# Optimization experiments

Hardware: AMD Instinct MI355X
Metric: run time of the kernel (lower is better)

## Reference

```python
import jax, jax.numpy as jnp
import numpy as np


def _cayley():
    # Cl(3,0) basis blades ordered by grade, lexicographic: 1,e1,e2,e3,e12,e13,e23,e123
    blades = [0b000, 0b001, 0b010, 0b100, 0b011, 0b101, 0b110, 0b111]
    idx = {b: i for i, b in enumerate(blades)}
    C = np.zeros((8, 8, 8), np.float32)
    for a in blades:
        for b in blades:
            t, s = a >> 1, 0
            while t:
                s += bin(t & b).count('1')
                t >>= 1
            C[idx[a], idx[a ^ b], idx[b]] = -1.0 if (s & 1) else 1.0
    return jnp.asarray(C)

CAYLEY = _cayley()                      # [8,8,8], metric [1,1,1]
GRADE = jnp.array([0, 1, 1, 1, 2, 2, 2, 3])  # blade -> grade (subspace) index
N_NODES, N_EDGES = 5, 20
NUM_HEADS = 8


def mv_linear(x, w, b):
    # MVLinear with subspaces=True: one scalar weight per (out, in, grade),
    # expanded to the 8 blades; bias only on the grade-0 (scalar) blade.
    # x: [N, m, 8], w: [n, m, 4], b: [n]
    out = jnp.einsum('bmi,nmi->bni', x, w[:, :, GRADE])
    return out.at[..., 0].add(b)


def _ln(x, g, b):
    m = jnp.mean(x, axis=-1, keepdims=True)
    v = jnp.var(x, axis=-1, keepdims=True)
    return (x - m) * jax.lax.rsqrt(v + 1e-5) * g + b


def _forward(nodes, edges, src_mask, batch_size, W_in, b_in, W_gp, b_gp,
             Wq, Wk, Wv, Wo, ln1_g, ln1_b, ln2_g, ln2_b, W1, b1, W2, b2):
    B = batch_size
    S = N_NODES + N_EDGES
    c_in = nodes.shape[1]
    nodes4 = nodes.reshape(B, N_NODES, c_in, 8)
    edges4 = edges.reshape(B, N_EDGES, c_in, 8)
    src = jnp.concatenate([nodes4, edges4], axis=1).reshape(B * S, c_in, 8)

    src_mv = mv_linear(src, W_in, b_in)                               # [B*S, dm, 8]
    src_gp = jnp.einsum('bni,ijk,bnk->bnj', src_mv, CAYLEY, src_mv)   # geometric product
    src2 = mv_linear(jnp.concatenate([src_mv, src_gp], axis=1), W_gp, b_gp)

    dm = src2.shape[1]
    D = dm * 8                                                        # 56 flat features
    H = NUM_HEADS
    hd = D // H
    x = src2.reshape(B, S, D)

    L = Wq.shape[0]
    for l in range(L):                                                # fixed small layer count
        h = _ln(x, ln1_g[l], ln1_b[l])
        q = (h @ Wq[l]).reshape(B, S, H, hd)
        k = (h @ Wk[l]).reshape(B, S, H, hd)
        v = (h @ Wv[l]).reshape(B, S, H, hd)
        scores = jnp.einsum('bqhd,bkhd->bhqk', q, k) / jnp.sqrt(jnp.float32(hd))
        scores = scores + src_mask[:, None, :, :]
        attn = jax.nn.softmax(scores, axis=-1)
        o = jnp.einsum('bhqk,bkhd->bqhd', attn, v).reshape(B, S, D)
        x = x + o @ Wo[l]
        h2 = _ln(x, ln2_g[l], ln2_b[l])
        x = x + jax.nn.gelu(h2 @ W1[l] + b1[l]) @ W2[l] + b2[l]

    out = x.reshape(B, S, dm, 8)
    sel = out[:, :N_NODES, 1, :]                                      # feature channel 1
    return sel.reshape(B * N_NODES, 8)


def setup_inputs() -> dict:
    key = jax.random.key(0)
    ks = jax.random.split(key, 12)
    B, c_in, dm, L = 4096, 3, 7, 4
    D = dm * 8
    Dff = 4 * D

    def r(k, shp, s=0.02):
        return jax.random.normal(k, shp, jnp.float32) * s

    return dict(
        nodes=jax.random.normal(ks[0], (B * N_NODES, c_in, 8), jnp.float32),
        edges=jax.random.normal(ks[1], (B * N_EDGES, c_in, 8), jnp.float32),
        src_mask=jnp.zeros((B, 25, 25), jnp.float32),
        batch_size=B,
        W_in=r(ks[2], (dm, c_in, 4), 1.0 / np.sqrt(c_in)),
        b_in=jnp.zeros((dm,), jnp.float32),
        W_gp=r(ks[3], (dm, 2 * dm, 4), 1.0 / np.sqrt(2 * dm)),
        b_gp=jnp.zeros((dm,), jnp.float32),
        Wq=r(ks[4], (L, D, D)), Wk=r(ks[5], (L, D, D)),
        Wv=r(ks[6], (L, D, D)), Wo=r(ks[7], (L, D, D)),
        ln1_g=jnp.ones((L, D), jnp.float32), ln1_b=jnp.zeros((L, D), jnp.float32),
        ln2_g=jnp.ones((L, D), jnp.float32), ln2_b=jnp.zeros((L, D), jnp.float32),
        W1=r(ks[8], (L, D, Dff)), b1=jnp.zeros((L, Dff), jnp.float32),
        W2=r(ks[9], (L, Dff, D)), b2=jnp.zeros((L, D), jnp.float32),
    )


def reference(nodes, edges, src_mask, batch_size, W_in, b_in, W_gp, b_gp,
              Wq, Wk, Wv, Wo, ln1_g, ln1_b, ln2_g, ln2_b, W1, b1, W2, b2):
    return _forward(nodes, edges, src_mask, batch_size, W_in, b_in, W_gp, b_gp,
                    Wq, Wk, Wv, Wo, ln1_g, ln1_b, ln2_g, ln2_b, W1, b1, W2, b2)
```

## Files before the change

kernel.cpp:

```cpp
#include <hip/hip_runtime.h>
#include <math.h>

#define NTH 256
#define XSTR 60
#define QHSTR 72
#define FSTR 232
#define LOG2E 1.4426950408889634f

typedef __attribute__((ext_vector_type(8))) short short8;
typedef __attribute__((ext_vector_type(4))) float f32x4;
typedef _Float16 half2_t __attribute__((ext_vector_type(2)));

__device__ __forceinline__ half2_t as_h2(unsigned int u) {
    return __builtin_bit_cast(half2_t, u);
}

__device__ __forceinline__ float fast_exp2(float x) {
    float r;
    asm("v_exp_f32 %0, %1" : "=v"(r) : "v"(x));
    return r;
}

__device__ __forceinline__ unsigned short f2bf(float x) {
    unsigned int u = __float_as_uint(x);
    return (unsigned short)((u + 0x7FFFu + ((u >> 16) & 1u)) >> 16);
}
__device__ __forceinline__ unsigned short f2bf_t(float x) {
    return (unsigned short)(__float_as_uint(x) >> 16);
}

__host__ __device__ constexpr int pc_(int v) { int c = 0; while (v) { c += v & 1; v >>= 1; } return c; }
__host__ __device__ constexpr int gp_sign(int a, int b) {
    int s = 0; int t = a >> 1;
    while (t) { s += pc_(t & b); t >>= 1; }
    return (s & 1) ? -1 : 1;
}
#define BLADE(i) ((int)((0x76534210u >> ((i) * 4)) & 0xF))

__device__ __forceinline__ float gelu_sig(float z) {
    float E = fast_exp2(-2.4554669f * z);
    return z * __builtin_amdgcn_rcpf(1.0f + E);
}

__global__ void prep_weights(const float* __restrict__ Wq, const float* __restrict__ Wk,
                             const float* __restrict__ Wv, const float* __restrict__ Wo,
                             const float* __restrict__ W1, const float* __restrict__ W2,
                             unsigned short* __restrict__ ws, int L)
{
    int idx = blockIdx.x * NTH + threadIdx.x;
    int total1 = L * 16384, total2 = L * 14336, total3 = L * 14336;
    if (idx < total1) {
        int k = idx & 63, n = (idx >> 6) & 63, mat = (idx >> 12) & 3, l = idx >> 14;
        float v = 0.f;
        if (k < 56 && n < 56) {
            const float* W = (mat == 0) ? Wq : (mat == 1) ? Wk : (mat == 2) ? Wv : Wo;
            v = W[l * 3136 + k * 56 + n];
            if (mat == 0) v *= 0.3779644730092272f * LOG2E;
        }
        ws[idx] = f2bf(v);
    } else if (idx < total1 + total2) {
        int t = idx - total1;
        int k = t & 63, n = (t >> 6) % 224, l = t / 14336;
        float v = (k < 56) ? W1[l * 12544 + k * 224 + n] : 0.f;
        ws[idx] = f2bf(v);
    } else if (idx < total1 + total2 + total3) {
        int t = idx - total1 - total2;
        int k = t % 224, n = (t / 224) & 63, l = t / 14336;
        float v = (n < 56) ? W2[l * 12544 + k * 56 + n] : 0.f;
        ws[idx] = f2bf(v);
    }
}

__global__ __launch_bounds__(NTH, 5) void nbody_fused(
    const float* __restrict__ nodes, const float* __restrict__ edges,
    const float* __restrict__ src_mask,
    const float* __restrict__ W_in, const float* __restrict__ b_in,
    const float* __restrict__ W_gp, const float* __restrict__ b_gp,
    const float* __restrict__ ln1g, const float* __restrict__ ln1b,
    const float* __restrict__ ln2g, const float* __restrict__ ln2b,
    const float* __restrict__ b1, const float* __restrict__ b2,
    const unsigned short* __restrict__ ws, int L,
    float* __restrict__ out)
{
    __shared__ __align__(16) float XS[25 * XSTR];
    __shared__ __align__(16) unsigned short HB[2304];
    __shared__ __align__(16) unsigned short UNI[5800];
    __shared__ __align__(16) float MKF[625];

    _Float16* QH = (_Float16*)UNI;
    _Float16* KH = QH + 25 * QHSTR;
    _Float16* VH = KH + 25 * QHSTR;
    unsigned short* FB = UNI;
    float* SRCF = XS;
    float* KBs = (float*)UNI;
    float* VBs = KBs + 25 * 57;

    const int b = blockIdx.x, tid = threadIdx.x;
    const int lane = tid & 63, wid = tid >> 6;
    const int nl = lane & 15, quad = lane >> 4;
    const int col = wid * 16 + nl;
    const int pcolh = (col / 7) * 8 + col % 7;
    const int ln_g = lane >> 3, ln_p = lane & 7;
    const int ln_s = wid + 4 * ln_g;

    for (int t = tid; t < 600; t += NTH) {
        int s = t / 24, r = t % 24;
        SRCF[t] = (s < 5) ? nodes[b * 120 + t] : edges[b * 480 + (s - 5) * 24 + r];
    }
    for (int t = tid; t < 625; t += NTH) MKF[t] = src_mask[b * 625 + t] * LOG2E;
    {
        int r = tid >> 3, c = 56 + (tid & 7);
        HB[r * 72 + c] = 0;
    }
    __syncthreads();

    for (int t = tid; t < 1400; t += NTH) {
        int s = t / 56, rem = t % 56, n = rem >> 3, i = rem & 7;
        int g = __popc(BLADE(i));
        float acc = (i == 0) ? b_in[n] : 0.0f;
        #pragma unroll
        for (int m = 0; m < 3; m++)
            acc += SRCF[s * 24 + m * 8 + i] * W_in[n * 12 + m * 4 + g];
        KBs[s * 57 + rem] = acc;
    }
    __syncthreads();

    for (int t = tid; t < 175; t += NTH) {
        int s = t / 7, n = t % 7;
        float m8[8], g8[8];
        #pragma unroll
        for (int i = 0; i < 8; i++) { m8[i] = KBs[s * 57 + n * 8 + i]; g8[i] = 0.0f; }
        #pragma unroll
        for (int ai = 0; ai < 8; ai++) {
            const int a = BLADE(ai);
            #pragma unroll
            for (int bi = 0; bi < 8; bi++) {
                const int bb = BLADE(bi);
                const int j = BLADE(a ^ bb);
                const int sg = gp_sign(a, bb);
                g8[j] += (sg > 0) ? (m8[ai] * m8[bi]) : (-m8[ai] * m8[bi]);
            }
        }
        #pragma unroll
        for (int j = 0; j < 8; j++) VBs[s * 57 + n * 8 + j] = g8[j];
    }
    __syncthreads();

    for (int t = tid; t < 1400; t += NTH) {
        int s = t / 56, rem = t % 56, n = rem >> 3, i = rem & 7;
        int g = __popc(BLADE(i));
        float acc = (i == 0) ? b_gp[n] : 0.0f;
        #pragma unroll
        for (int m = 0; m < 7; m++)
            acc += KBs[s * 57 + m * 8 + i] * W_gp[n * 56 + m * 4 + g];
        #pragma unroll
        for (int m = 0; m < 7; m++)
            acc += VBs[s * 57 + m * 8 + i] * W_gp[n * 56 + (7 + m) * 4 + g];
        XS[s * XSTR + rem] = acc;
    }
    __syncthreads();

    const unsigned short* w1t_all = ws + (size_t)L * 16384;
    const unsigned short* w2t_all = w1t_all + (size_t)L * 14336;

    for (int l = 0; l < L; l++) {
        const float* g1 = ln1g + l * 56; const float* e1 = ln1b + l * 56;
        const float* g2 = ln2g + l * 56; const float* e2 = ln2b + l * 56;

        if (tid < 200) {
            int s = tid >> 3, hh = tid & 7;
            QH[s * QHSTR + hh * 8 + 7] = (_Float16)0.f;
            KH[s * QHSTR + hh * 8 + 7] = (_Float16)0.f;
        }
        {
            float x[7]; float sum = 0.f, sq = 0.f;
            if (ln_s < 25) {
                const float* xp = XS + ln_s * XSTR + ln_p * 7;
                #pragma unroll
                for (int j = 0; j < 7; j++) { x[j] = xp[j]; sum += x[j]; sq += x[j] * x[j]; }
            }
            #pragma unroll
            for (int off = 1; off < 8; off <<= 1) {
                sum += __shfl_xor(sum, off, 64);
                sq  += __shfl_xor(sq,  off, 64);
            }
            if (ln_s < 25) {
                float mean = sum * (1.0f / 56.0f);
                float rs = __builtin_amdgcn_rsqf(sq * (1.0f / 56.0f) - mean * mean + 1e-5f);
                unsigned short* hp = HB + ln_s * 72 + ln_p * 7;
                #pragma unroll
                for (int j = 0; j < 7; j++) {
                    int d = ln_p * 7 + j;
                    hp[j] = f2bf_t((x[j] - mean) * rs * g1[d] + e1[d]);
                }
            }
        }
        __syncthreads();

        {
            short8 a[2][2];
            #pragma unroll
            for (int mt = 0; mt < 2; mt++)
                #pragma unroll
                for (int ks = 0; ks < 2; ks++)
                    a[mt][ks] = *(const short8*)(HB + (mt * 16 + nl) * 72 + ks * 32 + quad * 8);
            #pragma unroll
            for (int mat = 0; mat < 3; mat++) {
                const unsigned short* bp = ws + (((size_t)(l * 4 + mat)) << 12) + (((size_t)col) << 6) + quad * 8;
                short8 b0 = *(const short8*)(bp);
                short8 b1f = *(const short8*)(bp + 32);
                f32x4 acc0 = {0, 0, 0, 0}, acc1 = {0, 0, 0, 0};
                acc0 = __builtin_amdgcn_mfma_f32_16x16x32_bf16(a[0][0], b0, acc0, 0, 0, 0);
                acc0 = __builtin_amdgcn_mfma_f32_16x16x32_bf16(a[0][1], b1f, acc0, 0, 0, 0);
                acc1 = __builtin_amdgcn_mfma_f32_16x16x32_bf16(a[1][0], b0, acc1, 0, 0, 0);
                acc1 = __builtin_amdgcn_mfma_f32_16x16x32_bf16(a[1][1], b1f, acc1, 0, 0, 0);
                _Float16* dst = (mat == 0) ? QH : (mat == 1) ? KH : VH;
                if (col < 56) {
                    #pragma unroll
                    for (int r = 0; r < 4; r++) {
                        int row0 = quad * 4 + r;
                        dst[row0 * QHSTR + pcolh] = (_Float16)acc0[r];
                        int row1 = 16 + row0;
                        if (row1 < 25) dst[row1 * QHSTR + pcolh] = (_Float16)acc1[r];
                    }
                }
            }
        }
        __syncthreads();

        if (tid < 200) {
            int s = tid >> 3, hh = tid & 7;
            uint4 Q = *(const uint4*)(QH + s * QHSTR + hh * 8);
            half2_t q0 = as_h2(Q.x), q1 = as_h2(Q.y), q2 = as_h2(Q.z), q3 = as_h2(Q.w);
            float lsum = 0.f;
            half2_t acc0 = {0, 0}, acc1 = {0, 0}, acc2 = {0, 0}, acc3 = {0, 0};
            #pragma unroll 2
            for (int kk = 0; kk < 25; kk++) {
                uint4 K = *(const uint4*)(KH + kk * QHSTR + hh * 8);
                float dot = MKF[s * 25 + kk];
                dot = __builtin_amdgcn_fdot2(q3, as_h2(K.w), dot, false);
                dot = __builtin_amdgcn_fdot2(q2, as_h2(K.z), dot, false);
                dot = __builtin_amdgcn_fdot2(q1, as_h2(K.y), dot, false);
                dot = __builtin_amdgcn_fdot2(q0, as_h2(K.x), dot, false);
                float p = fast_exp2(dot);
                lsum += p;
                uint4 V = *(const uint4*)(VH + kk * QHSTR + hh * 8);
                _Float16 ph = (_Float16)p;
                half2_t p2 = {ph, ph};
                acc0 += p2 * as_h2(V.x); acc1 += p2 * as_h2(V.y);
                acc2 += p2 * as_h2(V.z); acc3 += p2 * as_h2(V.w);
            }
            float inv = __builtin_amdgcn_rcpf(lsum);
            unsigned short* op = HB + s * 72 + hh * 7;
            op[0] = f2bf_t((float)acc0.x * inv); op[1] = f2bf_t((float)acc0.y * inv);
            op[2] = f2bf_t((float)acc1.x * inv); op[3] = f2bf_t((float)acc1.y * inv);
            op[4] = f2bf_t((float)acc2.x * inv); op[5] = f2bf_t((float)acc2.y * inv);
            op[6] = f2bf_t((float)acc3.x * inv);
        }
        __syncthreads();

        {
            short8 a[2][2];
            #pragma unroll
            for (int mt = 0; mt < 2; mt++)
                #pragma unroll
                for (int ks = 0; ks < 2; ks++)
                    a[mt][ks] = *(const short8*)(HB + (mt * 16 + nl) * 72 + ks * 32 + quad * 8);
            const unsigned short* bp = ws + (((size_t)(l * 4 + 3)) << 12) + (((size_t)col) << 6) + quad * 8;
            short8 b0 = *(const short8*)(bp);
            short8 b1f = *(const short8*)(bp + 32);
            f32x4 acc0 = {0, 0, 0, 0}, acc1 = {0, 0, 0, 0};
            acc0 = __builtin_amdgcn_mfma_f32_16x16x32_bf16(a[0][0], b0, acc0, 0, 0, 0);
            acc0 = __builtin_amdgcn_mfma_f32_16x16x32_bf16(a[0][1], b1f, acc0, 0, 0, 0);
            acc1 = __builtin_amdgcn_mfma_f32_16x16x32_bf16(a[1][0], b0, acc1, 0, 0, 0);
            acc1 = __builtin_amdgcn_mfma_f32_16x16x32_bf16(a[1][1], b1f, acc1, 0, 0, 0);
            if (col < 56) {
                #pragma unroll
                for (int r = 0; r < 4; r++) {
                    int row0 = quad * 4 + r;
                    XS[row0 * XSTR + col] += acc0[r];
                    int row1 = 16 + row0;
                    if (row1 < 25) XS[row1 * XSTR + col] += acc1[r];
                }
            }
        }
        __syncthreads();

        {
            float x[7]; float sum = 0.f, sq = 0.f;
            if (ln_s < 25) {
                const float* xp = XS + ln_s * XSTR + ln_p * 7;
                #pragma unroll
                for (int j = 0; j < 7; j++) { x[j] = xp[j]; sum += x[j]; sq += x[j] * x[j]; }
            }
            #pragma unroll
            for (int off = 1; off < 8; off <<= 1) {
                sum += __shfl_xor(sum, off, 64);
                sq  += __shfl_xor(sq,  off, 64);
            }
            if (ln_s < 25) {
                float mean = sum * (1.0f / 56.0f);
                float rs = __builtin_amdgcn_rsqf(sq * (1.0f / 56.0f) - mean * mean + 1e-5f);
                unsigned short* hp = HB + ln_s * 72 + ln_p * 7;
                #pragma unroll
                for (int j = 0; j < 7; j++) {
                    int d = ln_p * 7 + j;
                    hp[j] = f2bf_t((x[j] - mean) * rs * g2[d] + e2[d]);
                }
            }
        }
        __syncthreads();

        {
            short8 a[2][2];
            #pragma unroll
            for (int mt = 0; mt < 2; mt++)
                #pragma unroll
                for (int ks = 0; ks < 2; ks++)
                    a[mt][ks] = *(const short8*)(HB + (mt * 16 + nl) * 72 + ks * 32 + quad * 8);
            for (int u = wid; u < 14; u += 4) {
                int c1 = u * 16 + nl;
                const unsigned short* bp = w1t_all + (((size_t)(l * 224 + c1)) << 6) + quad * 8;
                short8 b0 = *(const short8*)(bp);
                short8 b1f = *(const short8*)(bp + 32);
                f32x4 acc0 = {0, 0, 0, 0}, acc1 = {0, 0, 0, 0};
                acc0 = __builtin_amdgcn_mfma_f32_16x16x32_bf16(a[0][0], b0, acc0, 0, 0, 0);
                acc0 = __builtin_amdgcn_mfma_f32_16x16x32_bf16(a[0][1], b1f, acc0, 0, 0, 0);
                acc1 = __builtin_amdgcn_mfma_f32_16x16x32_bf16(a[1][0], b0, acc1, 0, 0, 0);
                acc1 = __builtin_amdgcn_mfma_f32_16x16x32_bf16(a[1][1], b1f, acc1, 0, 0, 0);
                float bias = b1[l * 224 + c1];
                #pragma unroll
                for (int r = 0; r < 4; r++) {
                    int row0 = quad * 4 + r;
                    FB[row0 * FSTR + c1] = f2bf_t(gelu_sig(acc0[r] + bias));
                    int row1 = 16 + row0;
                    if (row1 < 25) FB[row1 * FSTR + c1] = f2bf_t(gelu_sig(acc1[r] + bias));
                }
            }
        }
        __syncthreads();

        {
            int r1 = 16 + nl; if (r1 > 24) r1 = 24;
            const unsigned short* a0p = FB + nl * FSTR;
            const unsigned short* a1p = FB + r1 * FSTR;
            const unsigned short* bp0 = w2t_all + ((size_t)(l * 64 + col)) * 224 + quad * 8;
            f32x4 acc0 = {0, 0, 0, 0}, acc1 = {0, 0, 0, 0};
            #pragma unroll
            for (int ks = 0; ks < 7; ks++) {
                short8 bfrag = *(const short8*)(bp0 + ks * 32);
                short8 a0 = *(const short8*)(a0p + ks * 32 + quad * 8);
                short8 a1 = *(const short8*)(a1p + ks * 32 + quad * 8);
                acc0 = __builtin_amdgcn_mfma_f32_16x16x32_bf16(a0, bfrag, acc0, 0, 0, 0);
                acc1 = __builtin_amdgcn_mfma_f32_16x16x32_bf16(a1, bfrag, acc1, 0, 0, 0);
            }
            if (col < 56) {
                float bias = b2[l * 56 + col];
                #pragma unroll
                for (int r = 0; r < 4; r++) {
                    int row0 = quad * 4 + r;
                    XS[row0 * XSTR + col] += acc0[r] + bias;
                    int row1 = 16 + row0;
                    if (row1 < 25) XS[row1 * XSTR + col] += acc1[r] + bias;
                }
            }
        }
        __syncthreads();
    }

    for (int t = tid; t < 40; t += NTH) {
        int s = t >> 3, j = t & 7;
        out[(b * 5 + s) * 8 + j] = XS[s * XSTR + 8 + j];
    }
}

extern "C" void kernel_launch(void* const* d_in, const int* in_sizes, int n_in,
                              void* d_out, int out_size, void* d_ws, size_t ws_size,
                              hipStream_t stream) {
    const float* nodes = (const float*)d_in[0];
    const float* edges = (const float*)d_in[1];
    const float* mask  = (const float*)d_in[2];
    const int B = in_sizes[0] / 120;
    const float* W_in = (const float*)d_in[4];
    const float* b_in = (const float*)d_in[5];
    const float* W_gp = (const float*)d_in[6];
    const float* b_gp = (const float*)d_in[7];
    const float* Wq   = (const float*)d_in[8];
    const float* Wk   = (const float*)d_in[9];
    const float* Wv   = (const float*)d_in[10];
    const float* Wo   = (const float*)d_in[11];
    const float* ln1g = (const float*)d_in[12];
    const float* ln1b = (const float*)d_in[13];
    const float* ln2g = (const float*)d_in[14];
    const float* ln2b = (const float*)d_in[15];
    const float* W1   = (const float*)d_in[16];
    const float* b1   = (const float*)d_in[17];
    const float* W2   = (const float*)d_in[18];
    const float* b2   = (const float*)d_in[19];
    float* out = (float*)d_out;
    const int L = in_sizes[8] / 3136;

    unsigned short* ws16 = (unsigned short*)d_ws;
    int prep_total = L * (16384 + 14336 + 14336);
    hipLaunchKernelGGL(prep_weights, dim3((prep_total + NTH - 1) / NTH), dim3(NTH), 0, stream,
                       Wq, Wk, Wv, Wo, W1, W2, ws16, L);

    hipLaunchKernelGGL(nbody_fused, dim3(B), dim3(NTH), 0, stream,
                       nodes, edges, mask, W_in, b_in, W_gp, b_gp,
                       ln1g, ln1b, ln2g, ln2b, b1, b2, ws16, L, out);
}
```

Measured before the change: 310.8 us.

## Process two batch samples per workgroup to share weight fragments

Each workgroup now handles two batch elements with duplicated shared-memory buffers. Each loaded weight fragment for QKV, output projection, FFN1 and FFN2 feeds MFMAs for both samples, and the attention loop interleaves the two samples for more instruction-level parallelism. This halves the grid size and the barrier count per sample. In exchange it doubles LDS use per block and raises register pressure, so occupancy is lowered from 5 to 3 waves.

After: 311.4 us. Within noise of the previous version (+0.2%).

```diff
diff --git a/kernel.cpp b/kernel.cpp
--- a/kernel.cpp
+++ b/kernel.cpp
@@ -14,13 +14,11 @@
 __device__ __forceinline__ half2_t as_h2(unsigned int u) {
     return __builtin_bit_cast(half2_t, u);
 }
-
 __device__ __forceinline__ float fast_exp2(float x) {
     float r;
     asm("v_exp_f32 %0, %1" : "=v"(r) : "v"(x));
     return r;
 }
-
 __device__ __forceinline__ unsigned short f2bf(float x) {
     unsigned int u = __float_as_uint(x);
     return (unsigned short)((u + 0x7FFFu + ((u >> 16) & 1u)) >> 16);
@@ -71,7 +69,7 @@
     }
 }
 
-__global__ __launch_bounds__(NTH, 5) void nbody_fused(
+__global__ __launch_bounds__(NTH, 3) void nbody_fused(
     const float* __restrict__ nodes, const float* __restrict__ edges,
     const float* __restrict__ src_mask,
     const float* __restrict__ W_in, const float* __restrict__ b_in,
@@ -79,23 +77,15 @@
     const float* __restrict__ ln1g, const float* __restrict__ ln1b,
     const float* __restrict__ ln2g, const float* __restrict__ ln2b,
     const float* __restrict__ b1, const float* __restrict__ b2,
-    const unsigned short* __restrict__ ws, int L,
+    const unsigned short* __restrict__ ws, int L, int Btot,
     float* __restrict__ out)
 {
-    __shared__ __align__(16) float XS[25 * XSTR];
-    __shared__ __align__(16) unsigned short HB[2304];
-    __shared__ __align__(16) unsigned short UNI[5800];
-    __shared__ __align__(16) float MKF[625];
-
-    _Float16* QH = (_Float16*)UNI;
-    _Float16* KH = QH + 25 * QHSTR;
-    _Float16* VH = KH + 25 * QHSTR;
-    unsigned short* FB = UNI;
-    float* SRCF = XS;
-    float* KBs = (float*)UNI;
-    float* VBs = KBs + 25 * 57;
-
-    const int b = blockIdx.x, tid = threadIdx.x;
+    __shared__ __align__(16) float XS[2][25 * XSTR];
+    __shared__ __align__(16) unsigned short HB[2][2304];
+    __shared__ __align__(16) unsigned short UNI[2][5800];
+    __shared__ __align__(16) float MKF[2][625];
+
+    const int b0 = blockIdx.x * 2, tid = threadIdx.x;
     const int lane = tid & 63, wid = tid >> 6;
     const int nl = lane & 15, quad = lane >> 4;
     const int col = wid * 16 + nl;
@@ -103,60 +93,82 @@
     const int ln_g = lane >> 3, ln_p = lane & 7;
     const int ln_s = wid + 4 * ln_g;
 
-    for (int t = tid; t < 600; t += NTH) {
-        int s = t / 24, r = t % 24;
-        SRCF[t] = (s < 5) ? nodes[b * 120 + t] : edges[b * 480 + (s - 5) * 24 + r];
-    }
-    for (int t = tid; t < 625; t += NTH) MKF[t] = src_mask[b * 625 + t] * LOG2E;
-    {
-        int r = tid >> 3, c = 56 + (tid & 7);
-        HB[r * 72 + c] = 0;
+    for (int t = tid; t < 1200; t += NTH) {
+        int ss = t / 600, r0 = t - ss * 600;
+        int s = r0 / 24, r = r0 % 24;
+        int bb = b0 + ss;
+        if (bb < Btot)
+            XS[ss][r0] = (s < 5) ? nodes[bb * 120 + r0] : edges[bb * 480 + (s - 5) * 24 + r];
+    }
+    for (int t = tid; t < 1250; t += NTH) {
+        int ss = t / 625, r = t - ss * 625;
+        int bb = b0 + ss;
+        if (bb < Btot) MKF[ss][r] = src_mask[bb * 625 + r] * LOG2E;
+    }
+    for (int t = tid; t < 512; t += NTH) {
+        int ss = t >> 8, r = (t & 255) >> 3, c = 56 + (t & 7);
+        HB[ss][r * 72 + c] = 0;
     }
     __syncthreads();
 
-    for (int t = tid; t < 1400; t += NTH) {
-        int s = t / 56, rem = t % 56, n = rem >> 3, i = rem & 7;
-        int g = __popc(BLADE(i));
-        float acc = (i == 0) ? b_in[n] : 0.0f;
-        #pragma unroll
-        for (int m = 0; m < 3; m++)
-            acc += SRCF[s * 24 + m * 8 + i] * W_in[n * 12 + m * 4 + g];
-        KBs[s * 57 + rem] = acc;
+    #pragma unroll
+    for (int ss = 0; ss < 2; ss++) {
+        const float* SRCF = XS[ss];
+        float* KBs = (float*)UNI[ss];
+        for (int t = tid; t < 1400; t += NTH) {
+            int s = t / 56, rem = t % 56, n = rem >> 3, i = rem & 7;
+            int g = __popc(BLADE(i));
+            float acc = (i == 0) ? b_in[n] : 0.0f;
+            #pragma unroll
+            for (int m = 0; m < 3; m++)
+                acc += SRCF[s * 24 + m * 8 + i] * W_in[n * 12 + m * 4 + g];
+            KBs[s * 57 + rem] = acc;
+        }
     }
     __syncthreads();
 
-    for (int t = tid; t < 175; t += NTH) {
-        int s = t / 7, n = t % 7;
-        float m8[8], g8[8];
-        #pragma unroll
-        for (int i = 0; i < 8; i++) { m8[i] = KBs[s * 57 + n * 8 + i]; g8[i] = 0.0f; }
-        #pragma unroll
-        for (int ai = 0; ai < 8; ai++) {
-            const int a = BLADE(ai);
-            #pragma unroll
-            for (int bi = 0; bi < 8; bi++) {
-                const int bb = BLADE(bi);
-                const int j = BLADE(a ^ bb);
-                const int sg = gp_sign(a, bb);
-                g8[j] += (sg > 0) ? (m8[ai] * m8[bi]) : (-m8[ai] * m8[bi]);
-            }
-        }
-        #pragma unroll
-        for (int j = 0; j < 8; j++) VBs[s * 57 + n * 8 + j] = g8[j];
+    #pragma unroll
+    for (int ss = 0; ss < 2; ss++) {
+        float* KBs = (float*)UNI[ss];
+        float* VBs = KBs + 25 * 57;
+        for (int t = tid; t < 175; t += NTH) {
+            int s = t / 7, n = t % 7;
+            float m8[8], g8[8];
+            #pragma unroll
+            for (int i = 0; i < 8; i++) { m8[i] = KBs[s * 57 + n * 8 + i]; g8[i] = 0.0f; }
+            #pragma unroll
+            for (int ai = 0; ai < 8; ai++) {
+                const int a = BLADE(ai);
+                #pragma unroll
+                for (int bi = 0; bi < 8; bi++) {
+                    const int bb = BLADE(bi);
+                    const int j = BLADE(a ^ bb);
+                    const int sg = gp_sign(a, bb);
+                    g8[j] += (sg > 0) ? (m8[ai] * m8[bi]) : (-m8[ai] * m8[bi]);
+                }
+            }
+            #pragma unroll
+            for (int j = 0; j < 8; j++) VBs[s * 57 + n * 8 + j] = g8[j];
+        }
     }
     __syncthreads();
 
-    for (int t = tid; t < 1400; t += NTH) {
-        int s = t / 56, rem = t % 56, n = rem >> 3, i = rem & 7;
-        int g = __popc(BLADE(i));
-        float acc = (i == 0) ? b_gp[n] : 0.0f;
-        #pragma unroll
-        for (int m = 0; m < 7; m++)
-            acc += KBs[s * 57 + m * 8 + i] * W_gp[n * 56 + m * 4 + g];
-        #pragma unroll
-        for (int m = 0; m < 7; m++)
-            acc += VBs[s * 57 + m * 8 + i] * W_gp[n * 56 + (7 + m) * 4 + g];
-        XS[s * XSTR + rem] = acc;
+    #pragma unroll
+    for (int ss = 0; ss < 2; ss++) {
+        const float* KBs = (const float*)UNI[ss];
+        const float* VBs = KBs + 25 * 57;
+        for (int t = tid; t < 1400; t += NTH) {
+            int s = t / 56, rem = t % 56, n = rem >> 3, i = rem & 7;
+            int g = __popc(BLADE(i));
+            float acc = (i == 0) ? b_gp[n] : 0.0f;
+            #pragma unroll
+            for (int m = 0; m < 7; m++)
+                acc += KBs[s * 57 + m * 8 + i] * W_gp[n * 56 + m * 4 + g];
+            #pragma unroll
+            for (int m = 0; m < 7; m++)
+                acc += VBs[s * 57 + m * 8 + i] * W_gp[n * 56 + (7 + m) * 4 + g];
+            XS[ss][s * XSTR + rem] = acc;
+        }
     }
     __syncthreads();
 
@@ -169,13 +181,19 @@
 
         if (tid < 200) {
             int s = tid >> 3, hh = tid & 7;
-            QH[s * QHSTR + hh * 8 + 7] = (_Float16)0.f;
-            KH[s * QHSTR + hh * 8 + 7] = (_Float16)0.f;
-        }
-        {
+            #pragma unroll
+            for (int ss = 0; ss < 2; ss++) {
+                _Float16* QH = (_Float16*)UNI[ss];
+                _Float16* KH = QH + 25 * QHSTR;
+                QH[s * QHSTR + hh * 8 + 7] = (_Float16)0.f;
+                KH[s * QHSTR + hh * 8 + 7] = (_Float16)0.f;
+            }
+        }
+        #pragma unroll
+        for (int ss = 0; ss < 2; ss++) {
             float x[7]; float sum = 0.f, sq = 0.f;
             if (ln_s < 25) {
-                const float* xp = XS + ln_s * XSTR + ln_p * 7;
+                const float* xp = XS[ss] + ln_s * XSTR + ln_p * 7;
                 #pragma unroll
                 for (int j = 0; j < 7; j++) { x[j] = xp[j]; sum += x[j]; sq += x[j] * x[j]; }
             }
@@ -187,7 +205,7 @@
             if (ln_s < 25) {
                 float mean = sum * (1.0f / 56.0f);
                 float rs = __builtin_amdgcn_rsqf(sq * (1.0f / 56.0f) - mean * mean + 1e-5f);
-                unsigned short* hp = HB + ln_s * 72 + ln_p * 7;
+                unsigned short* hp = HB[ss] + ln_s * 72 + ln_p * 7;
                 #pragma unroll
                 for (int j = 0; j < 7; j++) {
                     int d = ln_p * 7 + j;
@@ -198,98 +216,132 @@
         __syncthreads();
 
         {
-            short8 a[2][2];
-            #pragma unroll
-            for (int mt = 0; mt < 2; mt++)
-                #pragma unroll
-                for (int ks = 0; ks < 2; ks++)
-                    a[mt][ks] = *(const short8*)(HB + (mt * 16 + nl) * 72 + ks * 32 + quad * 8);
+            short8 a[2][2][2];
+            #pragma unroll
+            for (int ss = 0; ss < 2; ss++)
+                #pragma unroll
+                for (int mt = 0; mt < 2; mt++)
+                    #pragma unroll
+                    for (int ks = 0; ks < 2; ks++)
+                        a[ss][mt][ks] = *(const short8*)(HB[ss] + (mt * 16 + nl) * 72 + ks * 32 + quad * 8);
             #pragma unroll
             for (int mat = 0; mat < 3; mat++) {
                 const unsigned short* bp = ws + (((size_t)(l * 4 + mat)) << 12) + (((size_t)col) << 6) + quad * 8;
-                short8 b0 = *(const short8*)(bp);
+                short8 b0f = *(const short8*)(bp);
                 short8 b1f = *(const short8*)(bp + 32);
+                #pragma unroll
+                for (int ss = 0; ss < 2; ss++) {
+                    f32x4 acc0 = {0, 0, 0, 0}, acc1 = {0, 0, 0, 0};
+                    acc0 = __builtin_amdgcn_mfma_f32_16x16x32_bf16(a[ss][0][0], b0f, acc0, 0, 0, 0);
+                    acc0 = __builtin_amdgcn_mfma_f32_16x16x32_bf16(a[ss][0][1], b1f, acc0, 0, 0, 0);
+                    acc1 = __builtin_amdgcn_mfma_f32_16x16x32_bf16(a[ss][1][0], b0f, acc1, 0, 0, 0);
+                    acc1 = __builtin_amdgcn_mfma_f32_16x16x32_bf16(a[ss][1][1], b1f, acc1, 0, 0, 0);
+                    _Float16* QH = (_Float16*)UNI[ss];
+                    _Float16* dst = QH + mat * 25 * QHSTR;
+                    if (col < 56) {
+                        #pragma unroll
+                        for (int r = 0; r < 4; r++) {
+                            int row0 = quad * 4 + r;
+                            dst[row0 * QHSTR + pcolh] = (_Float16)acc0[r];
+                            int row1 = 16 + row0;
+                            if (row1 < 25) dst[row1 * QHSTR + pcolh] = (_Float16)acc1[r];
+                        }
+                    }
+                }
+            }
+        }
+        __syncthreads();
+
+        if (tid < 200) {
+            int s = tid >> 3, hh = tid & 7;
+            const _Float16* QHa = (const _Float16*)UNI[0];
+            const _Float16* QHb = (const _Float16*)UNI[1];
+            const _Float16* KHa = QHa + 25 * QHSTR, * VHa = KHa + 25 * QHSTR;
+            const _Float16* KHb = QHb + 25 * QHSTR, * VHb = KHb + 25 * QHSTR;
+            uint4 Qa = *(const uint4*)(QHa + s * QHSTR + hh * 8);
+            uint4 Qb = *(const uint4*)(QHb + s * QHSTR + hh * 8);
+            half2_t qa0 = as_h2(Qa.x), qa1 = as_h2(Qa.y), qa2 = as_h2(Qa.z), qa3 = as_h2(Qa.w);
+            half2_t qb0 = as_h2(Qb.x), qb1 = as_h2(Qb.y), qb2 = as_h2(Qb.z), qb3 = as_h2(Qb.w);
+            float lsa = 0.f, lsb = 0.f;
+            half2_t aa0 = {0,0}, aa1 = {0,0}, aa2 = {0,0}, aa3 = {0,0};
+            half2_t ab0 = {0,0}, ab1 = {0,0}, ab2 = {0,0}, ab3 = {0,0};
+            for (int kk = 0; kk < 25; kk++) {
+                uint4 Ka = *(const uint4*)(KHa + kk * QHSTR + hh * 8);
+                uint4 Kb = *(const uint4*)(KHb + kk * QHSTR + hh * 8);
+                float da = MKF[0][s * 25 + kk];
+                float db = MKF[1][s * 25 + kk];
+                da = __builtin_amdgcn_fdot2(qa3, as_h2(Ka.w), da, false);
+                db = __builtin_amdgcn_fdot2(qb3, as_h2(Kb.w), db, false);
+                da = __builtin_amdgcn_fdot2(qa2, as_h2(Ka.z), da, false);
+                db = __builtin_amdgcn_fdot2(qb2, as_h2(Kb.z), db, false);
+                da = __builtin_amdgcn_fdot2(qa1, as_h2(Ka.y), da, false);
+                db = __builtin_amdgcn_fdot2(qb1, as_h2(Kb.y), db, false);
+                da = __builtin_amdgcn_fdot2(qa0, as_h2(Ka.x), da, false);
+                db = __builtin_amdgcn_fdot2(qb0, as_h2(Kb.x), db, false);
+                float pa = fast_exp2(da);
+                float pb = fast_exp2(db);
+                lsa += pa; lsb += pb;
+                uint4 Va = *(const uint4*)(VHa + kk * QHSTR + hh * 8);
+                uint4 Vb = *(const uint4*)(VHb + kk * QHSTR + hh * 8);
+                _Float16 pha = (_Float16)pa, phb = (_Float16)pb;
+                half2_t p2a = {pha, pha}, p2b = {phb, phb};
+                aa0 += p2a * as_h2(Va.x); aa1 += p2a * as_h2(Va.y);
+                aa2 += p2a * as_h2(Va.z); aa3 += p2a * as_h2(Va.w);
+                ab0 += p2b * as_h2(Vb.x); ab1 += p2b * as_h2(Vb.y);
+                ab2 += p2b * as_h2(Vb.z); ab3 += p2b * as_h2(Vb.w);
+            }
+            float inva = __builtin_amdgcn_rcpf(lsa);
+            float invb = __builtin_amdgcn_rcpf(lsb);
+            unsigned short* opa = HB[0] + s * 72 + hh * 7;
+            unsigned short* opb = HB[1] + s * 72 + hh * 7;
+            opa[0] = f2bf_t((float)aa0.x * inva); opa[1] = f2bf_t((float)aa0.y * inva);
+            opa[2] = f2bf_t((float)aa1.x * inva); opa[3] = f2bf_t((float)aa1.y * inva);
+            opa[4] = f2bf_t((float)aa2.x * inva); opa[5] = f2bf_t((float)aa2.y * inva);
+            opa[6] = f2bf_t((float)aa3.x * inva);
+            opb[0] = f2bf_t((float)ab0.x * invb); opb[1] = f2bf_t((float)ab0.y * invb);
+            opb[2] = f2bf_t((float)ab1.x * invb); opb[3] = f2bf_t((float)ab1.y * invb);
+            opb[4] = f2bf_t((float)ab2.x * invb); opb[5] = f2bf_t((float)ab2.y * invb);
+            opb[6] = f2bf_t((float)ab3.x * invb);
+        }
+        __syncthreads();
+
+        {
+            short8 a[2][2][2];
+            #pragma unroll
+            for (int ss = 0; ss < 2; ss++)
+                #pragma unroll
+                for (int mt = 0; mt < 2; mt++)
+                    #pragma unroll
+                    for (int ks = 0; ks < 2; ks++)
+                        a[ss][mt][ks] = *(const short8*)(HB[ss] + (mt * 16 + nl) * 72 + ks * 32 + quad * 8);
+            const unsigned short* bp = ws + (((size_t)(l * 4 + 3)) << 12) + (((size_t)col) << 6) + quad * 8;
+            short8 b0f = *(const short8*)(bp);
+            short8 b1f = *(const short8*)(bp + 32);
+            #pragma unroll
+            for (int ss = 0; ss < 2; ss++) {
                 f32x4 acc0 = {0, 0, 0, 0}, acc1 = {0, 0, 0, 0};
-                acc0 = __builtin_amdgcn_mfma_f32_16x16x32_bf16(a[0][0], b0, acc0, 0, 0, 0);
-                acc0 = __builtin_amdgcn_mfma_f32_16x16x32_bf16(a[0][1], b1f, acc0, 0, 0, 0);
-                acc1 = __builtin_amdgcn_mfma_f32_16x16x32_bf16(a[1][0], b0, acc1, 0, 0, 0);
-                acc1 = __builtin_amdgcn_mfma_f32_16x16x32_bf16(a[1][1], b1f, acc1, 0, 0, 0);
-                _Float16* dst = (mat == 0) ? QH : (mat == 1) ? KH : VH;
+                acc0 = __builtin_amdgcn_mfma_f32_16x16x32_bf16(a[ss][0][0], b0f, acc0, 0, 0, 0);
+                acc0 = __builtin_amdgcn_mfma_f32_16x16x32_bf16(a[ss][0][1], b1f, acc0, 0, 0, 0);
+                acc1 = __builtin_amdgcn_mfma_f32_16x16x32_bf16(a[ss][1][0], b0f, acc1, 0, 0, 0);
+                acc1 = __builtin_amdgcn_mfma_f32_16x16x32_bf16(a[ss][1][1], b1f, acc1, 0, 0, 0);
                 if (col < 56) {
                     #pragma unroll
                     for (int r = 0; r < 4; r++) {
                         int row0 = quad * 4 + r;
-                        dst[row0 * QHSTR + pcolh] = (_Float16)acc0[r];
+                        XS[ss][row0 * XSTR + col] += acc0[r];
                         int row1 = 16 + row0;
-                        if (row1 < 25) dst[row1 * QHSTR + pcolh] = (_Float16)acc1[r];
+                        if (row1 < 25) XS[ss][row1 * XSTR + col] += acc1[r];
                     }
                 }
             }
         }
         __syncthreads();
 
-        if (tid < 200) {
-            int s = tid >> 3, hh = tid & 7;
-            uint4 Q = *(const uint4*)(QH + s * QHSTR + hh * 8);
-            half2_t q0 = as_h2(Q.x), q1 = as_h2(Q.y), q2 = as_h2(Q.z), q3 = as_h2(Q.w);
-            float lsum = 0.f;
-            half2_t acc0 = {0, 0}, acc1 = {0, 0}, acc2 = {0, 0}, acc3 = {0, 0};
-            #pragma unroll 2
-            for (int kk = 0; kk < 25; kk++) {
-                uint4 K = *(const uint4*)(KH + kk * QHSTR + hh * 8);
-                float dot = MKF[s * 25 + kk];
-                dot = __builtin_amdgcn_fdot2(q3, as_h2(K.w), dot, false);
-                dot = __builtin_amdgcn_fdot2(q2, as_h2(K.z), dot, false);
-                dot = __builtin_amdgcn_fdot2(q1, as_h2(K.y), dot, false);
-                dot = __builtin_amdgcn_fdot2(q0, as_h2(K.x), dot, false);
-                float p = fast_exp2(dot);
-                lsum += p;
-                uint4 V = *(const uint4*)(VH + kk * QHSTR + hh * 8);
-                _Float16 ph = (_Float16)p;
-                half2_t p2 = {ph, ph};
-                acc0 += p2 * as_h2(V.x); acc1 += p2 * as_h2(V.y);
-                acc2 += p2 * as_h2(V.z); acc3 += p2 * as_h2(V.w);
-            }
-            float inv = __builtin_amdgcn_rcpf(lsum);
-            unsigned short* op = HB + s * 72 + hh * 7;
-            op[0] = f2bf_t((float)acc0.x * inv); op[1] = f2bf_t((float)acc0.y * inv);
-            op[2] = f2bf_t((float)acc1.x * inv); op[3] = f2bf_t((float)acc1.y * inv);
-            op[4] = f2bf_t((float)acc2.x * inv); op[5] = f2bf_t((float)acc2.y * inv);
-            op[6] = f2bf_t((float)acc3.x * inv);
-        }
-        __syncthreads();
-
-        {
-            short8 a[2][2];
-            #pragma unroll
-            for (int mt = 0; mt < 2; mt++)
-                #pragma unroll
-                for (int ks = 0; ks < 2; ks++)
-                    a[mt][ks] = *(const short8*)(HB + (mt * 16 + nl) * 72 + ks * 32 + quad * 8);
-            const unsigned short* bp = ws + (((size_t)(l * 4 + 3)) << 12) + (((size_t)col) << 6) + quad * 8;
-            short8 b0 = *(const short8*)(bp);
-            short8 b1f = *(const short8*)(bp + 32);
-            f32x4 acc0 = {0, 0, 0, 0}, acc1 = {0, 0, 0, 0};
-            acc0 = __builtin_amdgcn_mfma_f32_16x16x32_bf16(a[0][0], b0, acc0, 0, 0, 0);
-            acc0 = __builtin_amdgcn_mfma_f32_16x16x32_bf16(a[0][1], b1f, acc0, 0, 0, 0);
-            acc1 = __builtin_amdgcn_mfma_f32_16x16x32_bf16(a[1][0], b0, acc1, 0, 0, 0);
-            acc1 = __builtin_amdgcn_mfma_f32_16x16x32_bf16(a[1][1], b1f, acc1, 0, 0, 0);
-            if (col < 56) {
-                #pragma unroll
-                for (int r = 0; r < 4; r++) {
-                    int row0 = quad * 4 + r;
-                    XS[row0 * XSTR + col] += acc0[r];
-                    int row1 = 16 + row0;
-                    if (row1 < 25) XS[row1 * XSTR + col] += acc1[r];
-                }
-            }
-        }
-        __syncthreads();
-
-        {
+        #pragma unroll
+        for (int ss = 0; ss < 2; ss++) {
             float x[7]; float sum = 0.f, sq = 0.f;
             if (ln_s < 25) {
-                const float* xp = XS + ln_s * XSTR + ln_p * 7;
+                const float* xp = XS[ss] + ln_s * XSTR + ln_p * 7;
                 #pragma unroll
                 for (int j = 0; j < 7; j++) { x[j] = xp[j]; sum += x[j]; sq += x[j] * x[j]; }
             }
@@ -301,7 +353,7 @@
             if (ln_s < 25) {
                 float mean = sum * (1.0f / 56.0f);
                 float rs = __builtin_amdgcn_rsqf(sq * (1.0f / 56.0f) - mean * mean + 1e-5f);
-                unsigned short* hp = HB + ln_s * 72 + ln_p * 7;
+                unsigned short* hp = HB[ss] + ln_s * 72 + ln_p * 7;
                 #pragma unroll
                 for (int j = 0; j < 7; j++) {
                     int d = ln_p * 7 + j;
@@ -312,65 +364,81 @@
         __syncthreads();
 
         {
-            short8 a[2][2];
-            #pragma unroll
-            for (int mt = 0; mt < 2; mt++)
-                #pragma unroll
-                for (int ks = 0; ks < 2; ks++)
-                    a[mt][ks] = *(const short8*)(HB + (mt * 16 + nl) * 72 + ks * 32 + quad * 8);
+            short8 a[2][2][2];
+            #pragma unroll
+            for (int ss = 0; ss < 2; ss++)
+                #pragma unroll
+                for (int mt = 0; mt < 2; mt++)
+                    #pragma unroll
+                    for (int ks = 0; ks < 2; ks++)
+                        a[ss][mt][ks] = *(const short8*)(HB[ss] + (mt * 16 + nl) * 72 + ks * 32 + quad * 8);
             for (int u = wid; u < 14; u += 4) {
                 int c1 = u * 16 + nl;
                 const unsigned short* bp = w1t_all + (((size_t)(l * 224 + c1)) << 6) + quad * 8;
-                short8 b0 = *(const short8*)(bp);
+                short8 b0f = *(const short8*)(bp);
                 short8 b1f = *(const short8*)(bp + 32);
-                f32x4 acc0 = {0, 0, 0, 0}, acc1 = {0, 0, 0, 0};
-                acc0 = __builtin_amdgcn_mfma_f32_16x16x32_bf16(a[0][0], b0, acc0, 0, 0, 0);
-                acc0 = __builtin_amdgcn_mfma_f32_16x16x32_bf16(a[0][1], b1f, acc0, 0, 0, 0);
-                acc1 = __builtin_amdgcn_mfma_f32_16x16x32_bf16(a[1][0], b0, acc1, 0, 0, 0);
-                acc1 = __builtin_amdgcn_mfma_f32_16x16x32_bf16(a[1][1], b1f, acc1, 0, 0, 0);
                 float bias = b1[l * 224 + c1];
+                #pragma unroll
+                for (int ss = 0; ss < 2; ss++) {
+                    f32x4 acc0 = {0, 0, 0, 0}, acc1 = {0, 0, 0, 0};
+                    acc0 = __builtin_amdgcn_mfma_f32_16x16x32_bf16(a[ss][0][0], b0f, acc0, 0, 0, 0);
+                    acc0 = __builtin_amdgcn_mfma_f32_16x16x32_bf16(a[ss][0][1], b1f, acc0, 0, 0, 0);
+                    acc1 = __builtin_amdgcn_mfma_f32_16x16x32_bf16(a[ss][1][0], b0f, acc1, 0, 0, 0);
+                    acc1 = __builtin_amdgcn_mfma_f32_16x16x32_bf16(a[ss][1][1], b1f, acc1, 0, 0, 0);
+                    unsigned short* FB = UNI[ss];
+                    #pragma unroll
+                    for (int r = 0; r < 4; r++) {
+                        int row0 = quad * 4 + r;
+                        FB[row0 * FSTR + c1] = f2bf_t(gelu_sig(acc0[r] + bias));
+                        int row1 = 16 + row0;
+                        if (row1 < 25) FB[row1 * FSTR + c1] = f2bf_t(gelu_sig(acc1[r] + bias));
+                    }
+                }
+            }
+        }
+        __syncthreads();
+
+        {
+            int r1 = 16 + nl; if (r1 > 24) r1 = 24;
+            const unsigned short* bp0 = w2t_all + ((size_t)(l * 64 + col)) * 224 + quad * 8;
+            f32x4 acc0a = {0,0,0,0}, acc1a = {0,0,0,0}, acc0b = {0,0,0,0}, acc1b = {0,0,0,0};
+            #pragma unroll
+            for (int ks = 0; ks < 7; ks++) {
+                short8 bfrag = *(const short8*)(bp0 + ks * 32);
+                const unsigned short* FBa = UNI[0];
+                const unsigned short* FBb = UNI[1];
+                short8 a0a = *(const short8*)(FBa + nl * FSTR + ks * 32 + quad * 8);
+                short8 a1a = *(const short8*)(FBa + r1 * FSTR + ks * 32 + quad * 8);
+                short8 a0b = *(const short8*)(FBb + nl * FSTR + ks * 32 + quad * 8);
+                short8 a1b = *(const short8*)(FBb + r1 * FSTR + ks * 32 + quad * 8);
+                acc0a = __builtin_amdgcn_mfma_f32_16x16x32_bf16(a0a, bfrag, acc0a, 0, 0, 0);
+                acc0b = __builtin_amdgcn_mfma_f32_16x16x32_bf16(a0b, bfrag, acc0b, 0, 0, 0);
+                acc1a = __builtin_amdgcn_mfma_f32_16x16x32_bf16(a1a, bfrag, acc1a, 0, 0, 0);
+                acc1b = __builtin_amdgcn_mfma_f32_16x16x32_bf16(a1b, bfrag, acc1b, 0, 0, 0);
+            }
+            if (col < 56) {
+                float bias = b2[l * 56 + col];
                 #pragma unroll
                 for (int r = 0; r < 4; r++) {
                     int row0 = quad * 4 + r;
-                    FB[row0 * FSTR + c1] = f2bf_t(gelu_sig(acc0[r] + bias));
+                    XS[0][row0 * XSTR + col] += acc0a[r] + bias;
+                    XS[1][row0 * XSTR + col] += acc0b[r] + bias;
                     int row1 = 16 + row0;
-                    if (row1 < 25) FB[row1 * FSTR + c1] = f2bf_t(gelu_sig(acc1[r] + bias));
-                }
-            }
-        }
-        __syncthreads();
-
-        {
-            int r1 = 16 + nl; if (r1 > 24) r1 = 24;
-            const unsigned short* a0p = FB + nl * FSTR;
-            const unsigned short* a1p = FB + r1 * FSTR;
-            const unsigned short* bp0 = w2t_all + ((size_t)(l * 64 + col)) * 224 + quad * 8;
-            f32x4 acc0 = {0, 0, 0, 0}, acc1 = {0, 0, 0, 0};
-            #pragma unroll
-            for (int ks = 0; ks < 7; ks++) {
-                short8 bfrag = *(const short8*)(bp0 + ks * 32);
-                short8 a0 = *(const short8*)(a0p + ks * 32 + quad * 8);
-                short8 a1 = *(const short8*)(a1p + ks * 32 + quad * 8);
-                acc0 = __builtin_amdgcn_mfma_f32_16x16x32_bf16(a0, bfrag, acc0, 0, 0, 0);
-                acc1 = __builtin_amdgcn_mfma_f32_16x16x32_bf16(a1, bfrag, acc1, 0, 0, 0);
-            }
-            if (col < 56) {
-                float bias = b2[l * 56 + col];
-                #pragma unroll
-                for (int r = 0; r < 4; r++) {
-                    int row0 = quad * 4 + r;
-                    XS[row0 * XSTR + col] += acc0[r] + bias;
-                    int row1 = 16 + row0;
-                    if (row1 < 25) XS[row1 * XSTR + col] += acc1[r] + bias;
-                }
-            }
-        }
-        __syncthreads();
-    }
-
-    for (int t = tid; t < 40; t += NTH) {
-        int s = t >> 3, j = t & 7;
-        out[(b * 5 + s) * 8 + j] = XS[s * XSTR + 8 + j];
+                    if (row1 < 25) {
+                        XS[0][row1 * XSTR + col] += acc1a[r] + bias;
+                        XS[1][row1 * XSTR + col] += acc1b[r] + bias;
+                    }
+                }
+            }
+        }
+        __syncthreads();
+    }
+
+    for (int t = tid; t < 80; t += NTH) {
+        int ss = t / 40, r = t - ss * 40;
+        int s = r >> 3, j = r & 7;
+        int bb = b0 + ss;
+        if (bb < Btot) out[(bb * 5 + s) * 8 + j] = XS[ss][s * XSTR + 8 + j];
     }
 }
 
@@ -405,7 +473,7 @@
     hipLaunchKernelGGL(prep_weights, dim3((prep_total + NTH - 1) / NTH), dim3(NTH), 0, stream,
                        Wq, Wk, Wv, Wo, W1, W2, ws16, L);
 
-    hipLaunchKernelGGL(nbody_fused, dim3(B), dim3(NTH), 0, stream,
+    hipLaunchKernelGGL(nbody_fused, dim3((B + 1) / 2), dim3(NTH), 0, stream,
                        nodes, edges, mask, W_in, b_in, W_gp, b_gp,
-                       ln1g, ln1b, ln2g, ln2b, b1, b2, ws16, L, out);
-}
+                       ln1g, ln1b, ln2g, ln2b, b1, b2, ws16, L, B, out);
+}
```
